# Performance work log

Measured on AMD Instinct MI355X. Metric: run time of the kernel, lower is better.

Reference implementation:

```python
import jax, jax.numpy as jnp
import numpy as np

N = 8192
SQUARE_SIZE = 10.0
NEIGHBOURHOOD = 1.0
THRESHOLD = 1.0
DECAY = 0.9


def setup_inputs() -> dict:
    key = jax.random.key(0)
    k1, k2, k3, k4 = jax.random.split(key, 4)
    # Random 2D topology on a square, as in SpikingLayer.__init__
    topo = jax.random.uniform(k1, (N, 2), dtype=jnp.float32) * SQUARE_SIZE
    # Pairwise squared distances without the [N,N,2] intermediate
    sq = jnp.sum(topo * topo, axis=1)  # [N]
    d2 = sq[:, None] + sq[None, :] - 2.0 * (topo @ topo.T)  # [N,N]
    mask = (d2 <= NEIGHBOURHOOD * NEIGHBOURHOOD).astype(jnp.float32)
    # Per-node weight rows, zeroed outside the neighbourhood radius
    W = jax.random.normal(k2, (N, N), dtype=jnp.float32) * mask
    # Random initial firing state (0/1) so dynamics are non-trivial
    f0 = (jax.random.uniform(k3, (N,)) > 0.5).astype(jnp.float32)
    v0 = jnp.zeros((N,), dtype=jnp.float32)
    x = jax.random.normal(k4, (N,), dtype=jnp.float32)  # unused, as in torch forward
    return {"W": W, "f0": f0, "v0": v0, "x": x, "num_steps": 64}


def reference(W, f0, v0, x, num_steps):
    # One scan step == one call to SpikingLayer.forward():
    #   node_x = W @ is_firing  (fused over all nodes)
    #   LIF update: v = decay*v + node_x; spike if v >= threshold; reset on spike
    def step(carry, _):
        v, f = carry
        u = W @ f                      # [N] weighted input from firing neighbours
        v = DECAY * v + u
        spike = v >= THRESHOLD         # bool [N]
        f_new = spike.astype(v.dtype)
        v = jnp.where(spike, 0.0, v)   # reset fired neurons
        return (v, f_new), f_new

    (_, _), firing_matrix = jax.lax.scan(step, (v0, f0), None, length=num_steps)
    return firing_matrix  # [num_steps, N], the accumulated firing_matrix
```

## Files before the change

### kernel.cpp

```cpp
#include <hip/hip_runtime.h>

#define NN 8192
#define STEPS 64
#define DECAYF 0.9f
#define THRESHF 1.0f
#define K_MAX 384
#define KITER 24

#define CBLOCKS 256
#define STHREADS 576

typedef unsigned long long u64;
typedef unsigned int u32;

__device__ __forceinline__ void pub_store(u64* p, u64 v) {
    __hip_atomic_store(p, v, __ATOMIC_RELAXED, __HIP_MEMORY_SCOPE_AGENT);
}
__device__ __forceinline__ u64 pub_load(const u64* p) {
    return __hip_atomic_load(p, __ATOMIC_RELAXED, __HIP_MEMORY_SCOPE_AGENT);
}

__global__ __launch_bounds__(256) void extract_ell(
        const float* __restrict__ W,
        u64* __restrict__ pk) {
    const int wave = threadIdx.x >> 6;
    const int lane = threadIdx.x & 63;
    const int row  = blockIdx.x * 4 + wave;
    const float4* wr4 = (const float4*)(W + (size_t)row * NN);
    u64* pr = pk + (size_t)row * K_MAX;
    const u64 lmask = (1ull << lane) - 1ull;

    int base = 0;
    for (int c4 = lane; c4 < NN / 4; c4 += 64) {
        float4 w = wr4[c4];
        const int col0 = c4 * 4;
        #pragma unroll
        for (int comp = 0; comp < 4; ++comp) {
            float val = (comp == 0) ? w.x : (comp == 1) ? w.y
                      : (comp == 2) ? w.z : w.w;
            u64 m = __ballot(val != 0.0f);
            if (val != 0.0f) {
                int idx = base + __popcll(m & lmask);
                if (idx < K_MAX)
                    pr[idx] = ((u64)(u32)(col0 + comp) << 32)
                            | (u64)__float_as_uint(val);
            }
            base += __popcll(m);
        }
    }
    const int cap = (base < K_MAX) ? base : K_MAX;
    for (int j = cap + lane; j < K_MAX; j += 64) pr[j] = 0ull;
}

__global__ __launch_bounds__(STHREADS) void spiking_steps(
        const u64* __restrict__ pk,
        const float* __restrict__ f0,
        const float* __restrict__ v0,
        float* __restrict__ out,
        u64* __restrict__ fdata) {
    __shared__ u32 lds_fbits[2][CBLOCKS];
    __shared__ u32 lds_spike[8];
    __shared__ int lds_cnt[STEPS];
    __shared__ int lds_flag;

    const int tid  = threadIdx.x;
    const int wave = tid >> 6;
    const int lane = tid & 63;
    const int bid  = blockIdx.x;

    if (tid < STEPS) lds_cnt[tid] = 0;
    if (tid == 0) lds_flag = 0;

    if (wave == 0) {
        float f = (lane < 32) ? f0[bid * 32 + lane] : 0.0f;
        u64 m = __ballot(f != 0.0f);
        if (lane == 0)
            pub_store(&fdata[bid], (1ull << 32) | (u32)(m & 0xffffffffull));
    }
    __syncthreads();

    if (wave == 0) {
        for (int s = 0; s < STEPS; ++s) {
            const u64* slot = fdata + (size_t)(s & 1) * CBLOCKS;
            const u32 want = (u32)(s + 1);
            u32* fb = lds_fbits[s & 1];
            u32 pend = 0xFu;
            for (;;) {
                #pragma unroll
                for (int k = 0; k < 4; ++k) {
                    if ((pend >> k) & 1u) {
                        u64 w = pub_load(&slot[lane + 64 * k]);
                        if ((u32)(w >> 32) == want) {
                            fb[lane + 64 * k] = (u32)w;
                            pend &= ~(1u << k);
                        }
                    }
                }
                if (__all(pend == 0)) break;
            }
            if (lane == 0)
                __hip_atomic_store(&lds_flag, s + 1, __ATOMIC_RELEASE,
                                   __HIP_MEMORY_SCOPE_WORKGROUP);
        }
    } else {
        const int g    = wave - 1;
        const int rloc = g * 4 + (lane >> 4);
        const int row  = bid * 32 + rloc;
        const int l16  = lane & 15;

        u32 ecol[KITER]; float eval[KITER];
        const u64* pr = pk + (size_t)row * K_MAX;
        #pragma unroll
        for (int k = 0; k < KITER; ++k) {
            u64 p = pr[l16 + 16 * k];
            ecol[k] = (u32)(p >> 32);
            eval[k] = __uint_as_float((u32)p);
        }
        float vreg = v0[row];

        for (int s = 0; s < STEPS; ++s) {
            while (__hip_atomic_load(&lds_flag, __ATOMIC_ACQUIRE,
                                     __HIP_MEMORY_SCOPE_WORKGROUP) < s + 1) {}
            const u32* fb = lds_fbits[s & 1];

            double a0 = 0.0, a1 = 0.0, a2 = 0.0;
            #pragma unroll
            for (int k = 0; k < KITER; k += 3) {
                u32 c0 = ecol[k],     w0 = fb[c0 >> 5];
                u32 c1 = ecol[k + 1], w1 = fb[c1 >> 5];
                u32 c2 = ecol[k + 2], w2 = fb[c2 >> 5];
                a0 += (double)(((w0 >> (c0 & 31)) & 1u) ? eval[k]     : 0.0f);
                a1 += (double)(((w1 >> (c1 & 31)) & 1u) ? eval[k + 1] : 0.0f);
                a2 += (double)(((w2 >> (c2 & 31)) & 1u) ? eval[k + 2] : 0.0f);
            }
            double acc = (a0 + a1) + a2;
            #pragma unroll
            for (int m = 8; m >= 1; m >>= 1)
                acc += __shfl_xor(acc, m, 64);

            float u  = (float)acc;
            float vv = __fadd_rn(__fmul_rn(DECAYF, vreg), u);
            int fire = (vv >= THRESHF);
            vreg = fire ? 0.0f : vv;

            u64 bal = __ballot(fire);
            int old = -1;
            if (lane == 0) {
                u32 bits4 = ((u32)(bal       ) & 1u)
                          | (((u32)(bal >> 16) & 1u) << 1)
                          | (((u32)(bal >> 32) & 1u) << 2)
                          | (((u32)(bal >> 48) & 1u) << 3);
                __hip_atomic_store(&lds_spike[g], bits4, __ATOMIC_RELAXED,
                                   __HIP_MEMORY_SCOPE_WORKGROUP);
                old = __hip_atomic_fetch_add(&lds_cnt[s], 1, __ATOMIC_ACQ_REL,
                                             __HIP_MEMORY_SCOPE_WORKGROUP);
            }
            old = __shfl(old, 0, 64);
            if (old == 7) {
                u32 b = (lane < 8) ? ((lds_spike[lane] & 0xFu) << (4 * lane)) : 0u;
                b |= __shfl_xor(b, 1, 64);
                b |= __shfl_xor(b, 2, 64);
                b |= __shfl_xor(b, 4, 64);
                if (lane == 0)
                    pub_store(&fdata[(size_t)((s + 1) & 1) * CBLOCKS + bid],
                              ((u64)(u32)(s + 2) << 32) | b);
            }

            if (l16 == 0)
                out[(size_t)s * NN + row] = fire ? 1.0f : 0.0f;
        }
    }
}

extern "C" void kernel_launch(void* const* d_in, const int* in_sizes, int n_in,
                              void* d_out, int out_size, void* d_ws, size_t ws_size,
                              hipStream_t stream) {
    const float* W  = (const float*)d_in[0];
    const float* f0 = (const float*)d_in[1];
    const float* v0 = (const float*)d_in[2];
    float* out = (float*)d_out;

    u64* pk    = (u64*)d_ws;
    u64* fdata = pk + (size_t)NN * K_MAX;

    extract_ell<<<dim3(NN / 4), dim3(256), 0, stream>>>(W, pk);
    spiking_steps<<<dim3(CBLOCKS), dim3(STHREADS), 0, stream>>>(
        pk, f0, v0, out, fdata);
}
```

Measured before the change: 612.9 us.

## Pad per-block mailboxes to separate cache lines, back off polling, prefix-scan ELL extraction

Each block's published spike word now sits 16 u64 apart (128 bytes), so the mailboxes no longer share cache lines and a store from one block does not disturb lines other blocks are polling. The polling wave sleeps briefly between failed polls to cut memory traffic from spinning. ELL extraction swaps four ballots per float4 for a single shuffle-based prefix sum over per-lane nonzero counts. The trade-offs are more workspace footprint, wider-strided poll loads, and possibly added wakeup latency on each step handoff.

```diff
diff --git a/kernel.cpp b/kernel.cpp
--- a/kernel.cpp
+++ b/kernel.cpp
@@ -9,6 +9,7 @@
 
 #define CBLOCKS 256
 #define STHREADS 576
+#define MBSTRIDE 16
 
 typedef unsigned long long u64;
 typedef unsigned int u32;
@@ -28,25 +29,34 @@
     const int row  = blockIdx.x * 4 + wave;
     const float4* wr4 = (const float4*)(W + (size_t)row * NN);
     u64* pr = pk + (size_t)row * K_MAX;
-    const u64 lmask = (1ull << lane) - 1ull;
 
     int base = 0;
     for (int c4 = lane; c4 < NN / 4; c4 += 64) {
         float4 w = wr4[c4];
         const int col0 = c4 * 4;
+        int nz0 = (w.x != 0.0f), nz1 = (w.y != 0.0f),
+            nz2 = (w.z != 0.0f), nz3 = (w.w != 0.0f);
+        int cnt = nz0 + nz1 + nz2 + nz3;
+
+        int incl = cnt;
         #pragma unroll
-        for (int comp = 0; comp < 4; ++comp) {
-            float val = (comp == 0) ? w.x : (comp == 1) ? w.y
-                      : (comp == 2) ? w.z : w.w;
-            u64 m = __ballot(val != 0.0f);
-            if (val != 0.0f) {
-                int idx = base + __popcll(m & lmask);
-                if (idx < K_MAX)
-                    pr[idx] = ((u64)(u32)(col0 + comp) << 32)
-                            | (u64)__float_as_uint(val);
-            }
-            base += __popcll(m);
-        }
+        for (int d = 1; d < 64; d <<= 1) {
+            int n = __shfl_up(incl, d, 64);
+            if (lane >= d) incl += n;
+        }
+        int idx = base + (incl - cnt);
+        const int total = __shfl(incl, 63, 64);
+
+        if (nz0 && idx < K_MAX)
+            pr[idx++] = ((u64)(u32)(col0    ) << 32) | (u64)__float_as_uint(w.x);
+        if (nz1 && idx < K_MAX)
+            pr[idx++] = ((u64)(u32)(col0 + 1) << 32) | (u64)__float_as_uint(w.y);
+        if (nz2 && idx < K_MAX)
+            pr[idx++] = ((u64)(u32)(col0 + 2) << 32) | (u64)__float_as_uint(w.z);
+        if (nz3 && idx < K_MAX)
+            pr[idx++] = ((u64)(u32)(col0 + 3) << 32) | (u64)__float_as_uint(w.w);
+
+        base += total;
     }
     const int cap = (base < K_MAX) ? base : K_MAX;
     for (int j = cap + lane; j < K_MAX; j += 64) pr[j] = 0ull;
@@ -75,13 +85,14 @@
         float f = (lane < 32) ? f0[bid * 32 + lane] : 0.0f;
         u64 m = __ballot(f != 0.0f);
         if (lane == 0)
-            pub_store(&fdata[bid], (1ull << 32) | (u32)(m & 0xffffffffull));
+            pub_store(&fdata[(size_t)bid * MBSTRIDE],
+                      (1ull << 32) | (u32)(m & 0xffffffffull));
     }
     __syncthreads();
 
     if (wave == 0) {
         for (int s = 0; s < STEPS; ++s) {
-            const u64* slot = fdata + (size_t)(s & 1) * CBLOCKS;
+            const u64* slot = fdata + (size_t)(s & 1) * CBLOCKS * MBSTRIDE;
             const u32 want = (u32)(s + 1);
             u32* fb = lds_fbits[s & 1];
             u32 pend = 0xFu;
@@ -89,7 +100,7 @@
                 #pragma unroll
                 for (int k = 0; k < 4; ++k) {
                     if ((pend >> k) & 1u) {
-                        u64 w = pub_load(&slot[lane + 64 * k]);
+                        u64 w = pub_load(&slot[(size_t)(lane + 64 * k) * MBSTRIDE]);
                         if ((u32)(w >> 32) == want) {
                             fb[lane + 64 * k] = (u32)w;
                             pend &= ~(1u << k);
@@ -97,6 +108,7 @@
                     }
                 }
                 if (__all(pend == 0)) break;
+                __builtin_amdgcn_s_sleep(2);
             }
             if (lane == 0)
                 __hip_atomic_store(&lds_flag, s + 1, __ATOMIC_RELEASE,
@@ -162,7 +174,7 @@
                 b |= __shfl_xor(b, 2, 64);
                 b |= __shfl_xor(b, 4, 64);
                 if (lane == 0)
-                    pub_store(&fdata[(size_t)((s + 1) & 1) * CBLOCKS + bid],
+                    pub_store(&fdata[((size_t)((s + 1) & 1) * CBLOCKS + bid) * MBSTRIDE],
                               ((u64)(u32)(s + 2) << 32) | b);
             }
 
```

Measured after the change: 562.6 us. 1.09x faster.

## Split ELL extraction per half-row and pad spike mailboxes to cache lines

Applied to the files above, without the earlier changes.

The extraction kernel now gives each wave half a row, with a separate 192-slot ELL segment per half. This doubles the number of waves streaming the dense 256 MB weight matrix, aiming to raise memory parallelism in the bandwidth-bound preprocessing. The per-block spike mailboxes are spaced 128 bytes apart so producers and pollers no longer share cache lines. A short s_sleep is added in the polling loop to ease pressure on the memory system. The risks are segment overflow when one half has more than 192 nonzeros, and slightly slower wakeups from the sleep.

```diff
diff --git a/kernel.cpp b/kernel.cpp
--- a/kernel.cpp
+++ b/kernel.cpp
@@ -5,10 +5,12 @@
 #define DECAYF 0.9f
 #define THRESHF 1.0f
 #define K_MAX 384
+#define K_SEG 192
 #define KITER 24
 
 #define CBLOCKS 256
 #define STHREADS 576
+#define MBSTRIDE 16
 
 typedef unsigned long long u64;
 typedef unsigned int u32;
@@ -25,15 +27,19 @@
         u64* __restrict__ pk) {
     const int wave = threadIdx.x >> 6;
     const int lane = threadIdx.x & 63;
-    const int row  = blockIdx.x * 4 + wave;
-    const float4* wr4 = (const float4*)(W + (size_t)row * NN);
-    u64* pr = pk + (size_t)row * K_MAX;
+    const int hrow = blockIdx.x * 4 + wave;
+    const int row  = hrow >> 1;
+    const int half = hrow & 1;
+    const int cbase = half * (NN / 2);
+
+    const float4* wr4 = (const float4*)(W + (size_t)row * NN + cbase);
+    u64* pr = pk + (size_t)row * K_MAX + half * K_SEG;
     const u64 lmask = (1ull << lane) - 1ull;
 
     int base = 0;
-    for (int c4 = lane; c4 < NN / 4; c4 += 64) {
+    for (int c4 = lane; c4 < NN / 8; c4 += 64) {
         float4 w = wr4[c4];
-        const int col0 = c4 * 4;
+        const int col0 = cbase + c4 * 4;
         #pragma unroll
         for (int comp = 0; comp < 4; ++comp) {
             float val = (comp == 0) ? w.x : (comp == 1) ? w.y
@@ -41,15 +47,15 @@
             u64 m = __ballot(val != 0.0f);
             if (val != 0.0f) {
                 int idx = base + __popcll(m & lmask);
-                if (idx < K_MAX)
+                if (idx < K_SEG)
                     pr[idx] = ((u64)(u32)(col0 + comp) << 32)
                             | (u64)__float_as_uint(val);
             }
             base += __popcll(m);
         }
     }
-    const int cap = (base < K_MAX) ? base : K_MAX;
-    for (int j = cap + lane; j < K_MAX; j += 64) pr[j] = 0ull;
+    const int cap = (base < K_SEG) ? base : K_SEG;
+    for (int j = cap + lane; j < K_SEG; j += 64) pr[j] = 0ull;
 }
 
 __global__ __launch_bounds__(STHREADS) void spiking_steps(
@@ -75,13 +81,14 @@
         float f = (lane < 32) ? f0[bid * 32 + lane] : 0.0f;
         u64 m = __ballot(f != 0.0f);
         if (lane == 0)
-            pub_store(&fdata[bid], (1ull << 32) | (u32)(m & 0xffffffffull));
+            pub_store(&fdata[(size_t)bid * MBSTRIDE],
+                      (1ull << 32) | (u32)(m & 0xffffffffull));
     }
     __syncthreads();
 
     if (wave == 0) {
         for (int s = 0; s < STEPS; ++s) {
-            const u64* slot = fdata + (size_t)(s & 1) * CBLOCKS;
+            const u64* slot = fdata + (size_t)(s & 1) * CBLOCKS * MBSTRIDE;
             const u32 want = (u32)(s + 1);
             u32* fb = lds_fbits[s & 1];
             u32 pend = 0xFu;
@@ -89,7 +96,7 @@
                 #pragma unroll
                 for (int k = 0; k < 4; ++k) {
                     if ((pend >> k) & 1u) {
-                        u64 w = pub_load(&slot[lane + 64 * k]);
+                        u64 w = pub_load(&slot[(size_t)(lane + 64 * k) * MBSTRIDE]);
                         if ((u32)(w >> 32) == want) {
                             fb[lane + 64 * k] = (u32)w;
                             pend &= ~(1u << k);
@@ -97,6 +104,7 @@
                     }
                 }
                 if (__all(pend == 0)) break;
+                __builtin_amdgcn_s_sleep(2);
             }
             if (lane == 0)
                 __hip_atomic_store(&lds_flag, s + 1, __ATOMIC_RELEASE,
@@ -162,7 +170,7 @@
                 b |= __shfl_xor(b, 2, 64);
                 b |= __shfl_xor(b, 4, 64);
                 if (lane == 0)
-                    pub_store(&fdata[(size_t)((s + 1) & 1) * CBLOCKS + bid],
+                    pub_store(&fdata[((size_t)((s + 1) & 1) * CBLOCKS + bid) * MBSTRIDE],
                               ((u64)(u32)(s + 2) << 32) | b);
             }
 
@@ -183,7 +191,7 @@
     u64* pk    = (u64*)d_ws;
     u64* fdata = pk + (size_t)NN * K_MAX;
 
-    extract_ell<<<dim3(NN / 4), dim3(256), 0, stream>>>(W, pk);
+    extract_ell<<<dim3(NN * 2 / 4), dim3(256), 0, stream>>>(W, pk);
     spiking_steps<<<dim3(CBLOCKS), dim3(STHREADS), 0, stream>>>(
         pk, f0, v0, out, fdata);
 }
```

Measured after the change: 558.6 us. 1.1x faster.

## Fuse ELL extraction into persistent spiking kernel and pad mailbox slots

Applied to the files above, without the earlier changes.

Removes the separate extract_ell launch and its global ELL buffer. Each compute wave now scans its four W rows directly, compacts the nonzeros into an LDS staging buffer, and loads them into registers. Mailbox entries are spread out by a stride of 16 u64 so that blocks do not share cache lines, and the polling loop sleeps briefly between passes. The cost is that the dense 256 MB scan now runs on only 256 blocks of 8 compute waves, which may lower the achieved memory bandwidth compared with the 2048-block extraction kernel.

```diff
diff --git a/kernel.cpp b/kernel.cpp
--- a/kernel.cpp
+++ b/kernel.cpp
@@ -9,6 +9,7 @@
 
 #define CBLOCKS 256
 #define STHREADS 576
+#define MBSTRIDE 16
 
 typedef unsigned long long u64;
 typedef unsigned int u32;
@@ -20,44 +21,13 @@
     return __hip_atomic_load(p, __ATOMIC_RELAXED, __HIP_MEMORY_SCOPE_AGENT);
 }
 
-__global__ __launch_bounds__(256) void extract_ell(
+__global__ __launch_bounds__(STHREADS) void spiking_fused(
         const float* __restrict__ W,
-        u64* __restrict__ pk) {
-    const int wave = threadIdx.x >> 6;
-    const int lane = threadIdx.x & 63;
-    const int row  = blockIdx.x * 4 + wave;
-    const float4* wr4 = (const float4*)(W + (size_t)row * NN);
-    u64* pr = pk + (size_t)row * K_MAX;
-    const u64 lmask = (1ull << lane) - 1ull;
-
-    int base = 0;
-    for (int c4 = lane; c4 < NN / 4; c4 += 64) {
-        float4 w = wr4[c4];
-        const int col0 = c4 * 4;
-        #pragma unroll
-        for (int comp = 0; comp < 4; ++comp) {
-            float val = (comp == 0) ? w.x : (comp == 1) ? w.y
-                      : (comp == 2) ? w.z : w.w;
-            u64 m = __ballot(val != 0.0f);
-            if (val != 0.0f) {
-                int idx = base + __popcll(m & lmask);
-                if (idx < K_MAX)
-                    pr[idx] = ((u64)(u32)(col0 + comp) << 32)
-                            | (u64)__float_as_uint(val);
-            }
-            base += __popcll(m);
-        }
-    }
-    const int cap = (base < K_MAX) ? base : K_MAX;
-    for (int j = cap + lane; j < K_MAX; j += 64) pr[j] = 0ull;
-}
-
-__global__ __launch_bounds__(STHREADS) void spiking_steps(
-        const u64* __restrict__ pk,
         const float* __restrict__ f0,
         const float* __restrict__ v0,
         float* __restrict__ out,
         u64* __restrict__ fdata) {
+    __shared__ u64 lds_stage[8][K_MAX];
     __shared__ u32 lds_fbits[2][CBLOCKS];
     __shared__ u32 lds_spike[8];
     __shared__ int lds_cnt[STEPS];
@@ -75,13 +45,14 @@
         float f = (lane < 32) ? f0[bid * 32 + lane] : 0.0f;
         u64 m = __ballot(f != 0.0f);
         if (lane == 0)
-            pub_store(&fdata[bid], (1ull << 32) | (u32)(m & 0xffffffffull));
+            pub_store(&fdata[(size_t)bid * MBSTRIDE],
+                      (1ull << 32) | (u32)(m & 0xffffffffull));
     }
     __syncthreads();
 
     if (wave == 0) {
         for (int s = 0; s < STEPS; ++s) {
-            const u64* slot = fdata + (size_t)(s & 1) * CBLOCKS;
+            const u64* slot = fdata + (size_t)(s & 1) * CBLOCKS * MBSTRIDE;
             const u32 want = (u32)(s + 1);
             u32* fb = lds_fbits[s & 1];
             u32 pend = 0xFu;
@@ -89,7 +60,7 @@
                 #pragma unroll
                 for (int k = 0; k < 4; ++k) {
                     if ((pend >> k) & 1u) {
-                        u64 w = pub_load(&slot[lane + 64 * k]);
+                        u64 w = pub_load(&slot[(size_t)(lane + 64 * k) * MBSTRIDE]);
                         if ((u32)(w >> 32) == want) {
                             fb[lane + 64 * k] = (u32)w;
                             pend &= ~(1u << k);
@@ -97,24 +68,54 @@
                     }
                 }
                 if (__all(pend == 0)) break;
+                __builtin_amdgcn_s_sleep(2);
             }
             if (lane == 0)
                 __hip_atomic_store(&lds_flag, s + 1, __ATOMIC_RELEASE,
                                    __HIP_MEMORY_SCOPE_WORKGROUP);
         }
     } else {
-        const int g    = wave - 1;
-        const int rloc = g * 4 + (lane >> 4);
-        const int row  = bid * 32 + rloc;
-        const int l16  = lane & 15;
+        const int g   = wave - 1;
+        const int sub = lane >> 4;
+        const int l16 = lane & 15;
+        const int row = bid * 32 + g * 4 + sub;
+        const u64 lmask = (1ull << lane) - 1ull;
 
         u32 ecol[KITER]; float eval[KITER];
-        const u64* pr = pk + (size_t)row * K_MAX;
-        #pragma unroll
-        for (int k = 0; k < KITER; ++k) {
-            u64 p = pr[l16 + 16 * k];
-            ecol[k] = (u32)(p >> 32);
-            eval[k] = __uint_as_float((u32)p);
+        u64* st = lds_stage[g];
+
+        for (int r = 0; r < 4; ++r) {
+            const float4* wr4 =
+                (const float4*)(W + (size_t)(bid * 32 + g * 4 + r) * NN);
+            int base = 0;
+            for (int c4 = lane; c4 < NN / 4; c4 += 64) {
+                float4 w = wr4[c4];
+                const int col0 = c4 * 4;
+                #pragma unroll
+                for (int comp = 0; comp < 4; ++comp) {
+                    float val = (comp == 0) ? w.x : (comp == 1) ? w.y
+                              : (comp == 2) ? w.z : w.w;
+                    u64 m = __ballot(val != 0.0f);
+                    if (val != 0.0f) {
+                        int idx = base + __popcll(m & lmask);
+                        if (idx < K_MAX)
+                            st[idx] = ((u64)(u32)(col0 + comp) << 32)
+                                    | (u64)__float_as_uint(val);
+                    }
+                    base += __popcll(m);
+                }
+            }
+            const int cap = (base < K_MAX) ? base : K_MAX;
+            for (int j = cap + lane; j < K_MAX; j += 64) st[j] = 0ull;
+
+            if (sub == r) {
+                #pragma unroll
+                for (int k = 0; k < KITER; ++k) {
+                    u64 p = st[l16 + 16 * k];
+                    ecol[k] = (u32)(p >> 32);
+                    eval[k] = __uint_as_float((u32)p);
+                }
+            }
         }
         float vreg = v0[row];
 
@@ -162,7 +163,7 @@
                 b |= __shfl_xor(b, 2, 64);
                 b |= __shfl_xor(b, 4, 64);
                 if (lane == 0)
-                    pub_store(&fdata[(size_t)((s + 1) & 1) * CBLOCKS + bid],
+                    pub_store(&fdata[((size_t)((s + 1) & 1) * CBLOCKS + bid) * MBSTRIDE],
                               ((u64)(u32)(s + 2) << 32) | b);
             }
 
@@ -180,10 +181,8 @@
     const float* v0 = (const float*)d_in[2];
     float* out = (float*)d_out;
 
-    u64* pk    = (u64*)d_ws;
-    u64* fdata = pk + (size_t)NN * K_MAX;
+    u64* fdata = (u64*)d_ws;
 
-    extract_ell<<<dim3(NN / 4), dim3(256), 0, stream>>>(W, pk);
-    spiking_steps<<<dim3(CBLOCKS), dim3(STHREADS), 0, stream>>>(
-        pk, f0, v0, out, fdata);
+    spiking_fused<<<dim3(CBLOCKS), dim3(STHREADS), 0, stream>>>(
+        W, f0, v0, out, fdata);
 }
```

Result: faster. 581.8 us (-5.1%).
